# Performance work log

Hardware: AMD Instinct MI355X
Metric: run time of the kernel (lower is better)

Reference implementation:

```python
import jax, jax.numpy as jnp
import numpy as np

B, N, KD, VD, ID, H = 2, 2048, 1024, 1024, 1024, 16
HD = ID // H
SCALE = ID ** (-0.5)  # module quirk: scale uses inner_dim, not head_dim
EPS = 1e-5


def layernorm(x, g, b):
    mu = jnp.mean(x, axis=-1, keepdims=True)
    var = jnp.var(x, axis=-1, keepdims=True)
    return (x - mu) * jax.lax.rsqrt(var + EPS) * g + b


def setup_inputs() -> dict:
    key = jax.random.key(0)
    ks = jax.random.split(key, 12)
    d = {
        "keys": jax.random.normal(ks[0], (B, N, KD), jnp.float32),
        "values": jax.random.normal(ks[1], (B, N, VD), jnp.float32),
        "qk_norm_g": jnp.ones((KD,), jnp.float32),
        "qk_norm_b": jnp.zeros((KD,), jnp.float32),
        "value_norm_g": jnp.ones((VD,), jnp.float32),
        "value_norm_b": jnp.zeros((VD,), jnp.float32),
        "key_norm_g": jnp.ones((ID,), jnp.float32),
        "key_norm_b": jnp.zeros((ID,), jnp.float32),
        "query_norm_g": jnp.ones((ID,), jnp.float32),
        "query_norm_b": jnp.zeros((ID,), jnp.float32),
        "w_qk": jax.random.normal(ks[2], (KD, 2 * ID), jnp.float32) * (KD ** -0.5),
        "w_v": jax.random.normal(ks[3], (VD, ID), jnp.float32) * (VD ** -0.5),
        "w_out": jax.random.normal(ks[4], (ID, VD), jnp.float32) * (ID ** -0.5),
        "b_out": jnp.zeros((VD,), jnp.float32),
    }
    return d


def reference(keys, values, qk_norm_g, qk_norm_b, value_norm_g, value_norm_b,
              key_norm_g, key_norm_b, query_norm_g, query_norm_b,
              w_qk, w_v, w_out, b_out):
    keys = layernorm(keys, qk_norm_g, qk_norm_b)
    values = layernorm(values, value_norm_g, value_norm_b)
    qk = keys @ w_qk  # [B,N,2*ID]
    q, k = qk[..., :ID], qk[..., ID:]
    q = layernorm(q, query_norm_g, query_norm_b)
    k = layernorm(k, key_norm_g, key_norm_b)
    # b n (h d) -> b h n d
    q = q.reshape(B, N, H, HD).transpose(0, 2, 1, 3)
    k = k.reshape(B, N, H, HD).transpose(0, 2, 1, 3)
    v = (values @ w_v).reshape(B, N, H, HD).transpose(0, 2, 1, 3)
    dots = jnp.einsum('bhqd,bhkd->bhqk', q, k) * SCALE
    attn = jax.nn.softmax(dots, axis=-1)
    out = jnp.einsum('bhqk,bhkd->bhqd', attn, v)
    out = out.transpose(0, 2, 1, 3).reshape(B, N, ID)
    return out @ w_out + b_out
```

## Files before the change

### kernel.cpp

```cpp
#include <hip/hip_runtime.h>
#include <hip/hip_bf16.h>
#include <type_traits>


typedef __hip_bfloat16 bf16;
typedef __attribute__((ext_vector_type(8))) short bf16x8;
typedef __attribute__((ext_vector_type(4))) float f32x4;

#define MFMA_BF16(a, b, c) __builtin_amdgcn_mfma_f32_16x16x32_bf16((a), (b), (c), 0, 0, 0)

__device__ __forceinline__ float us2f(unsigned short u) {
  unsigned int v = ((unsigned int)u) << 16;
  return __builtin_bit_cast(float, v);
}

__device__ __forceinline__ unsigned pack_bf16x2(float a, float b) {
  union { __hip_bfloat162 h; unsigned u; } cv;
  cv.h = __float22bfloat162_rn(float2{a, b});
  return cv.u;
}

__device__ __forceinline__ unsigned pack_bf16x2_trunc(float a, float b) {
  return __builtin_amdgcn_perm(__builtin_bit_cast(unsigned, b),
                               __builtin_bit_cast(unsigned, a), 0x07060302u);
}

__device__ __forceinline__ void gl_lds16(const bf16* g, bf16* l) {
  __builtin_amdgcn_global_load_lds(
      (const __attribute__((address_space(1))) void*)g,
      (__attribute__((address_space(3))) void*)l, 16, 0, 0);
}

template <typename TIN>
__global__ __launch_bounds__(256) void ln2_kernel(
    const TIN* __restrict__ in0, const TIN* __restrict__ in1, int stride,
    const float* __restrict__ g0, const float* __restrict__ b0,
    const float* __restrict__ g1, const float* __restrict__ b1,
    bf16* __restrict__ out0, bf16* __restrict__ out1, int D,
    float sc0, float sc1)
{
  const int which = blockIdx.y;
  const TIN* in = which ? in1 : in0;
  const float* gamma = which ? g1 : g0;
  const float* beta = which ? b1 : b0;
  bf16* out = which ? out1 : out0;
  const float sc = which ? sc1 : sc0;
  const int row = blockIdx.x;
  const int t = threadIdx.x;
  float x0, x1, x2, x3;
  if constexpr (std::is_same_v<TIN, float>) {
    float4 u = *(const float4*)(in + (size_t)row * stride + t * 4);
    x0 = u.x; x1 = u.y; x2 = u.z; x3 = u.w;
  } else {
    ushort4 u = *(const ushort4*)(in + (size_t)row * stride + t * 4);
    x0 = us2f(u.x); x1 = us2f(u.y); x2 = us2f(u.z); x3 = us2f(u.w);
  }
  float s = x0 + x1 + x2 + x3;
  float s2 = x0 * x0 + x1 * x1 + x2 * x2 + x3 * x3;
#pragma unroll
  for (int m = 1; m < 64; m <<= 1) {
    s += __shfl_xor(s, m);
    s2 += __shfl_xor(s2, m);
  }
  __shared__ float red[10];
  const int w = t >> 6, lane = t & 63;
  if (lane == 0) { red[w] = s; red[4 + w] = s2; }
  __syncthreads();
  if (t == 0) {
    float S = red[0] + red[1] + red[2] + red[3];
    float S2 = red[4] + red[5] + red[6] + red[7];
    float mu = S / (float)D;
    float var = S2 / (float)D - mu * mu;
    red[8] = mu;
    red[9] = rsqrtf(var + 1e-5f);
  }
  __syncthreads();
  const float mu = red[8], rs = red[9];
  float4 g4 = *(const float4*)(gamma + t * 4);
  float4 b4 = *(const float4*)(beta + t * 4);
  uint2 o;
  o.x = pack_bf16x2(((x0 - mu) * rs * g4.x + b4.x) * sc, ((x1 - mu) * rs * g4.y + b4.y) * sc);
  o.y = pack_bf16x2(((x2 - mu) * rs * g4.z + b4.z) * sc, ((x3 - mu) * rs * g4.w + b4.w) * sc);
  *(uint2*)(out + (size_t)row * D + t * 4) = o;
}

__global__ __launch_bounds__(256) void transpose3_kernel(
    const float* __restrict__ s0, bf16* __restrict__ d0,
    const float* __restrict__ s1, bf16* __restrict__ d1,
    const float* __restrict__ s2, bf16* __restrict__ d2)
{
  const int z = blockIdx.z;
  if (z > 0 && blockIdx.x >= 16) return;
  const float* in = (z == 0) ? s0 : (z == 1) ? s1 : s2;
  bf16* out = (z == 0) ? d0 : (z == 1) ? d1 : d2;
  const int R = 1024, C = (z == 0) ? 2048 : 1024;
  __shared__ float tile[64][68];
  const int r0 = blockIdx.y * 64, c0 = blockIdx.x * 64;
  const int t = threadIdx.x;
  const int lr = t >> 2, lc = (t & 3) * 16;
  const float* src = in + (size_t)(r0 + lr) * C + (c0 + lc);
#pragma unroll
  for (int i = 0; i < 4; ++i) {
    float4 u = *(const float4*)(src + i * 4);
    tile[lr][lc + i * 4 + 0] = u.x;
    tile[lr][lc + i * 4 + 1] = u.y;
    tile[lr][lc + i * 4 + 2] = u.z;
    tile[lr][lc + i * 4 + 3] = u.w;
  }
  __syncthreads();
  __align__(16) bf16 tmp[16];
#pragma unroll
  for (int j = 0; j < 16; ++j) tmp[j] = __float2bfloat16(tile[lc + j][lr]);
  bf16* dst = out + (size_t)(c0 + lr) * R + (r0 + lc);
  *(bf16x8*)dst       = *(const bf16x8*)&tmp[0];
  *(bf16x8*)(dst + 8) = *(const bf16x8*)&tmp[8];
}

template <int BM, int BN, int TMODE, typename TOUT>
__global__ __launch_bounds__(256) void gemm_bt_kernel(
    const bf16* __restrict__ A, const bf16* __restrict__ Bt,
    const float* __restrict__ bias, TOUT* __restrict__ C,
    int M, int N, int K, int has_bias)
{
  constexpr int MT = BM / 32, NT = BN / 32;
  constexpr int ASL = BM / 32, BSL = BN / 32;
  constexpr int BUFE = (BM + BN) * 64;
  __shared__ __align__(16) bf16 smem[2 * BUFE];
  const int t = threadIdx.x;
  const int w = t >> 6, lane = t & 63, l15 = lane & 15, quad = lane >> 4;
  const int wy = w >> 1, wx = w & 1;
  const bf16* Ab = A + (size_t)blockIdx.y * BM * K;
  const bf16* Bb = Bt + (size_t)blockIdx.x * BN * K;
  f32x4 acc[MT][NT] = {};

  const bf16* aptr[ASL];
  const bf16* bptr[BSL];
#pragma unroll
  for (int i = 0; i < ASL; ++i) {
    int s = i * 256 + t, row = s >> 3, c = (s & 7) ^ (row & 7);
    aptr[i] = Ab + (size_t)row * K + (c << 3);
  }
#pragma unroll
  for (int i = 0; i < BSL; ++i) {
    int s = i * 256 + t, row = s >> 3, c = (s & 7) ^ (row & 7);
    bptr[i] = Bb + (size_t)row * K + (c << 3);
  }

  auto stage = [&](bf16* buf, int kc) {
#pragma unroll
    for (int i = 0; i < ASL; ++i)
      gl_lds16(aptr[i] + kc, buf + (i * 256 + t) * 8);
#pragma unroll
    for (int i = 0; i < BSL; ++i)
      gl_lds16(bptr[i] + kc, buf + BM * 64 + (i * 256 + t) * 8);
  };

  const int sw = (quad ^ (l15 & 7)) << 3;
  const int NK = K >> 6;

  stage(smem, 0);

  for (int kt = 0; kt < NK; ++kt) {
    const int cur = kt & 1;
    bf16* lA = smem + cur * BUFE;
    bf16* lB = lA + BM * 64;
    __builtin_amdgcn_s_barrier();
    if (kt + 1 < NK) {
      stage(smem + (cur ^ 1) * BUFE, (kt + 1) << 6);
      if constexpr (ASL + BSL == 8)
        asm volatile("s_waitcnt vmcnt(8)" ::: "memory");
      else
        asm volatile("s_waitcnt vmcnt(6)" ::: "memory");
    } else {
      asm volatile("s_waitcnt vmcnt(0)" ::: "memory");
    }
    __builtin_amdgcn_s_barrier();

#pragma unroll
    for (int h = 0; h < 2; ++h) {
      const int so = sw ^ (h << 5);
      bf16x8 af[MT], bfr[NT];
#pragma unroll
      for (int mt = 0; mt < MT; ++mt)
        af[mt] = *(const bf16x8*)&lA[(wy * (BM / 2) + mt * 16 + l15) * 64 + so];
#pragma unroll
      for (int nt = 0; nt < NT; ++nt)
        bfr[nt] = *(const bf16x8*)&lB[(wx * (BN / 2) + nt * 16 + l15) * 64 + so];
#pragma unroll
      for (int mt = 0; mt < MT; ++mt)
#pragma unroll
        for (int nt = 0; nt < NT; ++nt)
          acc[mt][nt] = MFMA_BF16(af[mt], bfr[nt], acc[mt][nt]);
    }
  }

  if constexpr (TMODE == 1) {
    static_assert(BM * BN == 8192, "TMODE1 epilogue assumes 8192 els/block");
    constexpr int STR = BM + 8;
    static_assert(BN * STR <= 2 * BUFE, "lOut must fit staging buffers");
    bf16* lOut = smem;
    __syncthreads();
#pragma unroll
    for (int mt = 0; mt < MT; ++mt)
#pragma unroll
      for (int nt = 0; nt < NT; ++nt) {
        const int d = wx * (BN / 2) + nt * 16 + l15;
        const int n = wy * (BM / 2) + mt * 16 + quad * 4;
        uint2 pk;
        pk.x = pack_bf16x2(acc[mt][nt][0], acc[mt][nt][1]);
        pk.y = pack_bf16x2(acc[mt][nt][2], acc[mt][nt][3]);
        *(uint2*)&lOut[d * STR + n] = pk;
      }
    __syncthreads();
    const int row0 = blockIdx.y * BM;
    const int bidx = row0 >> 11, n0 = row0 & 2047;
    const int col0 = blockIdx.x * BN;
    constexpr int CPR = BM / 32;
    const int d = t / CPR, off = (t % CPR) * 32;
    const bf16* srcp = &lOut[d * STR + off];
    bf16* g = (bf16*)C + ((size_t)(bidx << 10) + col0 + d) * 2048 + n0 + off;
#pragma unroll
    for (int j = 0; j < 4; ++j)
      *(bf16x8*)(g + j * 8) = *(const bf16x8*)(srcp + j * 8);
  } else {
    const int row_base = blockIdx.y * BM + wy * (BM / 2);
    const int col_base = blockIdx.x * BN + wx * (BN / 2);
#pragma unroll
    for (int mt = 0; mt < MT; ++mt)
#pragma unroll
      for (int nt = 0; nt < NT; ++nt) {
        const int col = col_base + nt * 16 + l15;
        const float bb = has_bias ? bias[col] : 0.0f;
#pragma unroll
        for (int r = 0; r < 4; ++r) {
          const int row = row_base + mt * 16 + quad * 4 + r;
          float v = acc[mt][nt][r] + bb;
          if constexpr (std::is_same_v<TOUT, bf16>)
            C[(size_t)row * N + col] = __float2bfloat16(v);
          else
            C[(size_t)row * N + col] = v;
        }
      }
  }
}

__global__ __launch_bounds__(256) void flash_kernel(
    const bf16* __restrict__ Q, const bf16* __restrict__ Km,
    const bf16* __restrict__ Vt, bf16* __restrict__ O)
{
  __shared__ __align__(16) bf16 smem[8192 + 8192 + 8192];
  bf16* lQ = smem;
  bf16* lKb = smem + 8192;
  bf16* lVb = smem + 16384;
  const int t = threadIdx.x;
  const int w = t >> 6, lane = t & 63, l15 = lane & 15, quad = lane >> 4;
  const int qt = blockIdx.x, bh = blockIdx.y;
  const int b = bh >> 4, h = bh & 15;
  const int qrow0 = b * 2048 + qt * 128;
  const bf16* qbase = Q + (size_t)qrow0 * 1024 + h * 64;
  const bf16* kbase = Km + ((size_t)(b * 2048)) * 1024 + h * 64;
  const bf16* vbase = Vt + ((size_t)(b * 1024 + h * 64)) * 2048;

  const int sr0 = t >> 3, sc0 = ((t & 7) ^ (sr0 & 7)) << 3;
  const int sr1 = (256 + t) >> 3, sc1 = (((256 + t) & 7) ^ (sr1 & 7)) << 3;
  const int gr0 = (sr0 & 0x23) | ((sr0 & 0x0C) << 1) | ((sr0 & 0x10) >> 2);
  const int gr1 = (sr1 & 0x23) | ((sr1 & 0x0C) << 1) | ((sr1 & 0x10) >> 2);
  const bf16* kp0 = kbase + gr0 * 1024 + sc0;
  const bf16* kp1 = kbase + gr1 * 1024 + sc1;
  const bf16* vp0 = vbase + sr0 * 2048 + sc0;
  const bf16* vp1 = vbase + sr1 * 2048 + sc1;

#pragma unroll
  for (int i = 0; i < 4; ++i) {
    int s = i * 256 + t;
    int row = s >> 3, c = (s & 7) ^ (row & 7);
    gl_lds16(qbase + (size_t)row * 1024 + (c << 3), lQ + s * 8);
  }
  gl_lds16(kp0, lKb + t * 8);
  gl_lds16(kp1, lKb + (256 + t) * 8);
  gl_lds16(vp0, lVb + t * 8);
  gl_lds16(vp1, lVb + (256 + t) * 8);
  asm volatile("s_waitcnt vmcnt(4)" ::: "memory");
  __builtin_amdgcn_s_barrier();

  const int sw = (quad ^ (l15 & 7)) << 3;
  bf16x8 qf[2][2];
#pragma unroll
  for (int mset = 0; mset < 2; ++mset) {
    const int row = w * 32 + mset * 16 + l15;
    qf[mset][0] = *(const bf16x8*)&lQ[row * 64 + sw];
    qf[mset][1] = *(const bf16x8*)&lQ[row * 64 + (sw ^ 32)];
  }

  f32x4 o_acc[4][2] = {};
  f32x4 l_vec[2] = {};

  for (int kt = 0; kt < 32; ++kt) {
    const int cur = kt & 1;
    bf16* lK = lKb + cur * 4096;
    bf16* lV = lVb + cur * 4096;
    bf16* lKn = lKb + (cur ^ 1) * 4096;
    bf16* lVn = lVb + (cur ^ 1) * 4096;

    __builtin_amdgcn_s_barrier();
    {
      const int ktn = (kt + 1) & 31;
      const int ko = ktn << 16;
      const int vo = ktn << 6;
      gl_lds16(kp0 + ko, lKn + t * 8);
      gl_lds16(kp1 + ko, lKn + (256 + t) * 8);
      gl_lds16(vp0 + vo, lVn + t * 8);
      gl_lds16(vp1 + vo, lVn + (256 + t) * 8);
    }
    asm volatile("s_waitcnt vmcnt(4)" ::: "memory");
    __builtin_amdgcn_s_barrier();

    bf16x8 kf[4][2];
#pragma unroll
    for (int nt = 0; nt < 4; ++nt) {
      kf[nt][0] = *(const bf16x8*)&lK[(nt * 16 + l15) * 64 + sw];
      kf[nt][1] = *(const bf16x8*)&lK[(nt * 16 + l15) * 64 + (sw ^ 32)];
    }

    bf16x8 pa[2][2];
#pragma unroll
    for (int mset = 0; mset < 2; ++mset) {
#pragma unroll
      for (int half = 0; half < 2; ++half) {
        f32x4 z0 = {}, z1 = {};
        z0 = MFMA_BF16(kf[2 * half + 0][0], qf[mset][0], z0);
        z0 = MFMA_BF16(kf[2 * half + 0][1], qf[mset][1], z0);
        z1 = MFMA_BF16(kf[2 * half + 1][0], qf[mset][0], z1);
        z1 = MFMA_BF16(kf[2 * half + 1][1], qf[mset][1], z1);
        f32x4 p0, p1;
#pragma unroll
        for (int r = 0; r < 4; ++r) {
          p0[r] = __builtin_amdgcn_exp2f(z0[r]);
          p1[r] = __builtin_amdgcn_exp2f(z1[r]);
        }
        l_vec[mset] += p0 + p1;
        union { unsigned u[4]; bf16x8 v; } cv;
        cv.u[0] = pack_bf16x2_trunc(p0[0], p0[1]);
        cv.u[1] = pack_bf16x2_trunc(p0[2], p0[3]);
        cv.u[2] = pack_bf16x2_trunc(p1[0], p1[1]);
        cv.u[3] = pack_bf16x2_trunc(p1[2], p1[3]);
        pa[mset][half] = cv.v;
      }
    }

    bf16x8 vf[4][2];
#pragma unroll
    for (int dt = 0; dt < 4; ++dt) {
      vf[dt][0] = *(const bf16x8*)&lV[(dt * 16 + l15) * 64 + sw];
      vf[dt][1] = *(const bf16x8*)&lV[(dt * 16 + l15) * 64 + (sw ^ 32)];
    }

    __builtin_amdgcn_s_setprio(1);
#pragma unroll
    for (int mset = 0; mset < 2; ++mset)
#pragma unroll
      for (int dt = 0; dt < 4; ++dt) {
        o_acc[dt][mset] = MFMA_BF16(vf[dt][0], pa[mset][0], o_acc[dt][mset]);
        o_acc[dt][mset] = MFMA_BF16(vf[dt][1], pa[mset][1], o_acc[dt][mset]);
      }
    __builtin_amdgcn_s_setprio(0);
  }

#pragma unroll
  for (int mset = 0; mset < 2; ++mset) {
    float tsum = l_vec[mset][0] + l_vec[mset][1] + l_vec[mset][2] + l_vec[mset][3];
    tsum += __shfl_xor(tsum, 16);
    tsum += __shfl_xor(tsum, 32);
    const float inv = 1.0f / tsum;
    const int m = qrow0 + w * 32 + mset * 16 + l15;
#pragma unroll
    for (int dt = 0; dt < 4; ++dt) {
      uint2 ok;
      ok.x = pack_bf16x2(o_acc[dt][mset][0] * inv, o_acc[dt][mset][1] * inv);
      ok.y = pack_bf16x2(o_acc[dt][mset][2] * inv, o_acc[dt][mset][3] * inv);
      *(uint2*)&O[(size_t)m * 1024 + h * 64 + dt * 16 + quad * 4] = ok;
    }
  }
}

extern "C" void kernel_launch(void* const* d_in, const int* in_sizes, int n_in,
                              void* d_out, int out_size, void* d_ws, size_t ws_size,
                              hipStream_t stream)
{
  (void)in_sizes; (void)n_in; (void)out_size; (void)ws_size;
  const float* keys   = (const float*)d_in[0];
  const float* values = (const float*)d_in[1];
  const float* qk_g   = (const float*)d_in[2];
  const float* qk_b   = (const float*)d_in[3];
  const float* val_g  = (const float*)d_in[4];
  const float* val_b  = (const float*)d_in[5];
  const float* key_g  = (const float*)d_in[6];
  const float* key_b  = (const float*)d_in[7];
  const float* qry_g  = (const float*)d_in[8];
  const float* qry_b  = (const float*)d_in[9];
  const float* w_qk   = (const float*)d_in[10];
  const float* w_v    = (const float*)d_in[11];
  const float* w_out  = (const float*)d_in[12];
  const float* b_out  = (const float*)d_in[13];
  float* out = (float*)d_out;

  const float CEXP = 0.03125f * 1.44269504f;

  char* ws = (char*)d_ws;
  const size_t MB = 1024 * 1024;
  bf16* keys_ln   = (bf16*)(ws + 0);
  bf16* values_ln = (bf16*)(ws + 8 * MB);
  bf16* qk        = (bf16*)(ws + 16 * MB);
  bf16* attn      = (bf16*)(ws + 16 * MB);
  bf16* vt        = (bf16*)(ws + 24 * MB);
  bf16* qln       = (bf16*)(ws + 32 * MB);
  bf16* kln       = (bf16*)(ws + 40 * MB);
  bf16* wqkT      = (bf16*)(ws + 48 * MB);
  bf16* wvT       = (bf16*)(ws + 52 * MB);
  bf16* woutT     = (bf16*)(ws + 54 * MB);

  ln2_kernel<float><<<dim3(4096, 2), 256, 0, stream>>>(
      keys, values, 1024, qk_g, qk_b, val_g, val_b, keys_ln, values_ln, 1024, 1.0f, 1.0f);
  transpose3_kernel<<<dim3(32, 16, 3), 256, 0, stream>>>(w_qk, wqkT, w_v, wvT, w_out, woutT);
  gemm_bt_kernel<128, 128, 0, bf16><<<dim3(16, 32), 256, 0, stream>>>(keys_ln, wqkT, nullptr, qk, 4096, 2048, 1024, 0);
  ln2_kernel<bf16><<<dim3(4096, 2), 256, 0, stream>>>(
      qk, qk + 1024, 2048, qry_g, qry_b, key_g, key_b, qln, kln, 1024, CEXP, 1.0f);
  gemm_bt_kernel<128, 64, 1, bf16><<<dim3(16, 32), 256, 0, stream>>>(values_ln, wvT, nullptr, vt, 4096, 1024, 1024, 0);
  flash_kernel<<<dim3(16, 32), 256, 0, stream>>>(qln, kln, vt, attn);
  gemm_bt_kernel<128, 64, 0, float><<<dim3(16, 32), 256, 0, stream>>>(attn, woutT, b_out, out, 4096, 1024, 1024, 1);
}
```

Measured before the change: 223.0 us.

## Merge prep launches and run QK and V projections in one dual GEMM

Folds the two input layernorms and the three weight transposes into a single prep kernel, and runs the QK and V projection GEMMs in one launch, with the V GEMM moved to 128x128 tiles. This cuts launch count and lets the smaller V GEMM fill the GPU alongside the QK GEMM. It also pins the barriers with sched_barrier so the compiler cannot move work across them, and repacks the workspace layout. Risks are heavier per-block shared memory in the merged kernels and schedule changes from the pinned barriers.

```diff
diff --git a/kernel.cpp b/kernel.cpp
--- a/kernel.cpp
+++ b/kernel.cpp
@@ -31,21 +31,17 @@
       (__attribute__((address_space(3))) void*)l, 16, 0, 0);
 }
 
+__device__ __forceinline__ void barrier_pinned() {
+  __builtin_amdgcn_s_barrier();
+  __builtin_amdgcn_sched_barrier(0);
+}
+
 template <typename TIN>
-__global__ __launch_bounds__(256) void ln2_kernel(
-    const TIN* __restrict__ in0, const TIN* __restrict__ in1, int stride,
-    const float* __restrict__ g0, const float* __restrict__ b0,
-    const float* __restrict__ g1, const float* __restrict__ b1,
-    bf16* __restrict__ out0, bf16* __restrict__ out1, int D,
-    float sc0, float sc1)
-{
-  const int which = blockIdx.y;
-  const TIN* in = which ? in1 : in0;
-  const float* gamma = which ? g1 : g0;
-  const float* beta = which ? b1 : b0;
-  bf16* out = which ? out1 : out0;
-  const float sc = which ? sc1 : sc0;
-  const int row = blockIdx.x;
+__device__ __forceinline__ void ln_core(
+    const TIN* __restrict__ in, const float* __restrict__ gamma,
+    const float* __restrict__ beta, bf16* __restrict__ out,
+    int stride, int D, float sc, int row, float* red)
+{
   const int t = threadIdx.x;
   float x0, x1, x2, x3;
   if constexpr (std::is_same_v<TIN, float>) {
@@ -62,7 +58,6 @@
     s += __shfl_xor(s, m);
     s2 += __shfl_xor(s2, m);
   }
-  __shared__ float red[10];
   const int w = t >> 6, lane = t & 63;
   if (lane == 0) { red[w] = s; red[4 + w] = s2; }
   __syncthreads();
@@ -84,18 +79,26 @@
   *(uint2*)(out + (size_t)row * D + t * 4) = o;
 }
 
-__global__ __launch_bounds__(256) void transpose3_kernel(
-    const float* __restrict__ s0, bf16* __restrict__ d0,
-    const float* __restrict__ s1, bf16* __restrict__ d1,
-    const float* __restrict__ s2, bf16* __restrict__ d2)
-{
-  const int z = blockIdx.z;
-  if (z > 0 && blockIdx.x >= 16) return;
-  const float* in = (z == 0) ? s0 : (z == 1) ? s1 : s2;
-  bf16* out = (z == 0) ? d0 : (z == 1) ? d1 : d2;
-  const int R = 1024, C = (z == 0) ? 2048 : 1024;
-  __shared__ float tile[64][68];
-  const int r0 = blockIdx.y * 64, c0 = blockIdx.x * 64;
+template <typename TIN>
+__global__ __launch_bounds__(256) void ln2_kernel(
+    const TIN* __restrict__ in0, const TIN* __restrict__ in1, int stride,
+    const float* __restrict__ g0, const float* __restrict__ b0,
+    const float* __restrict__ g1, const float* __restrict__ b1,
+    bf16* __restrict__ out0, bf16* __restrict__ out1, int D,
+    float sc0, float sc1)
+{
+  __shared__ float red[10];
+  const int which = blockIdx.y;
+  ln_core<TIN>(which ? in1 : in0, which ? g1 : g0, which ? b1 : b0,
+               which ? out1 : out0, stride, D, which ? sc1 : sc0,
+               blockIdx.x, red);
+}
+
+__device__ __forceinline__ void transpose_core(
+    const float* __restrict__ in, bf16* __restrict__ out, int C,
+    int r0, int c0, float (*tile)[68])
+{
+  const int R = 1024;
   const int t = threadIdx.x;
   const int lr = t >> 2, lc = (t & 3) * 16;
   const float* src = in + (size_t)(r0 + lr) * C + (c0 + lc);
@@ -116,21 +119,51 @@
   *(bf16x8*)(dst + 8) = *(const bf16x8*)&tmp[8];
 }
 
+__global__ __launch_bounds__(256) void prep_kernel(
+    const float* __restrict__ keys, const float* __restrict__ values,
+    const float* __restrict__ qk_g, const float* __restrict__ qk_b,
+    const float* __restrict__ val_g, const float* __restrict__ val_b,
+    bf16* __restrict__ keys_ln, bf16* __restrict__ values_ln,
+    const float* __restrict__ w_qk, bf16* __restrict__ wqkT,
+    const float* __restrict__ w_v, bf16* __restrict__ wvT,
+    const float* __restrict__ w_out, bf16* __restrict__ woutT)
+{
+  __shared__ float tile[64][68];
+  __shared__ float red[10];
+  const int bid = blockIdx.x;
+  if (bid < 8192) {
+    const int row = bid >> 1, which = bid & 1;
+    ln_core<float>(which ? values : keys, which ? val_g : qk_g,
+                   which ? val_b : qk_b, which ? values_ln : keys_ln,
+                   1024, 1024, 1.0f, row, red);
+  } else {
+    const int tz = bid - 8192;
+    if (tz < 512) {
+      transpose_core(w_qk, wqkT, 2048, (tz >> 5) * 64, (tz & 31) * 64, tile);
+    } else if (tz < 768) {
+      const int s = tz - 512;
+      transpose_core(w_v, wvT, 1024, (s >> 4) * 64, (s & 15) * 64, tile);
+    } else {
+      const int s = tz - 768;
+      transpose_core(w_out, woutT, 1024, (s >> 4) * 64, (s & 15) * 64, tile);
+    }
+  }
+}
+
 template <int BM, int BN, int TMODE, typename TOUT>
-__global__ __launch_bounds__(256) void gemm_bt_kernel(
+__device__ __forceinline__ void gemm_core(
     const bf16* __restrict__ A, const bf16* __restrict__ Bt,
     const float* __restrict__ bias, TOUT* __restrict__ C,
-    int M, int N, int K, int has_bias)
+    int N, int K, int has_bias, int bx, int by, bf16* smem)
 {
   constexpr int MT = BM / 32, NT = BN / 32;
   constexpr int ASL = BM / 32, BSL = BN / 32;
   constexpr int BUFE = (BM + BN) * 64;
-  __shared__ __align__(16) bf16 smem[2 * BUFE];
   const int t = threadIdx.x;
   const int w = t >> 6, lane = t & 63, l15 = lane & 15, quad = lane >> 4;
   const int wy = w >> 1, wx = w & 1;
-  const bf16* Ab = A + (size_t)blockIdx.y * BM * K;
-  const bf16* Bb = Bt + (size_t)blockIdx.x * BN * K;
+  const bf16* Ab = A + (size_t)by * BM * K;
+  const bf16* Bb = Bt + (size_t)bx * BN * K;
   f32x4 acc[MT][NT] = {};
 
   const bf16* aptr[ASL];
@@ -164,7 +197,7 @@
     const int cur = kt & 1;
     bf16* lA = smem + cur * BUFE;
     bf16* lB = lA + BM * 64;
-    __builtin_amdgcn_s_barrier();
+    barrier_pinned();
     if (kt + 1 < NK) {
       stage(smem + (cur ^ 1) * BUFE, (kt + 1) << 6);
       if constexpr (ASL + BSL == 8)
@@ -174,7 +207,7 @@
     } else {
       asm volatile("s_waitcnt vmcnt(0)" ::: "memory");
     }
-    __builtin_amdgcn_s_barrier();
+    barrier_pinned();
 
 #pragma unroll
     for (int h = 0; h < 2; ++h) {
@@ -195,7 +228,6 @@
   }
 
   if constexpr (TMODE == 1) {
-    static_assert(BM * BN == 8192, "TMODE1 epilogue assumes 8192 els/block");
     constexpr int STR = BM + 8;
     static_assert(BN * STR <= 2 * BUFE, "lOut must fit staging buffers");
     bf16* lOut = smem;
@@ -212,19 +244,24 @@
         *(uint2*)&lOut[d * STR + n] = pk;
       }
     __syncthreads();
-    const int row0 = blockIdx.y * BM;
+    const int row0 = by * BM;
     const int bidx = row0 >> 11, n0 = row0 & 2047;
-    const int col0 = blockIdx.x * BN;
+    const int col0 = bx * BN;
     constexpr int CPR = BM / 32;
-    const int d = t / CPR, off = (t % CPR) * 32;
-    const bf16* srcp = &lOut[d * STR + off];
-    bf16* g = (bf16*)C + ((size_t)(bidx << 10) + col0 + d) * 2048 + n0 + off;
-#pragma unroll
-    for (int j = 0; j < 4; ++j)
-      *(bf16x8*)(g + j * 8) = *(const bf16x8*)(srcp + j * 8);
+    constexpr int NITER = (BN * CPR) / 256;
+#pragma unroll
+    for (int it = 0; it < NITER; ++it) {
+      const int idx = it * 256 + t;
+      const int d = idx / CPR, off = (idx % CPR) * 32;
+      const bf16* srcp = &lOut[d * STR + off];
+      bf16* g = (bf16*)C + ((size_t)(bidx << 10) + col0 + d) * 2048 + n0 + off;
+#pragma unroll
+      for (int j = 0; j < 4; ++j)
+        *(bf16x8*)(g + j * 8) = *(const bf16x8*)(srcp + j * 8);
+    }
   } else {
-    const int row_base = blockIdx.y * BM + wy * (BM / 2);
-    const int col_base = blockIdx.x * BN + wx * (BN / 2);
+    const int row_base = by * BM + wy * (BM / 2);
+    const int col_base = bx * BN + wx * (BN / 2);
 #pragma unroll
     for (int mt = 0; mt < MT; ++mt)
 #pragma unroll
@@ -241,6 +278,33 @@
             C[(size_t)row * N + col] = v;
         }
       }
+  }
+}
+
+template <int BM, int BN, int TMODE, typename TOUT>
+__global__ __launch_bounds__(256) void gemm_bt_kernel(
+    const bf16* __restrict__ A, const bf16* __restrict__ Bt,
+    const float* __restrict__ bias, TOUT* __restrict__ C,
+    int N, int K, int has_bias)
+{
+  __shared__ __align__(16) bf16 smem[2 * (BM + BN) * 64];
+  gemm_core<BM, BN, TMODE, TOUT>(A, Bt, bias, C, N, K, has_bias,
+                                 blockIdx.x, blockIdx.y, smem);
+}
+
+__global__ __launch_bounds__(256) void gemm_dual_kernel(
+    const bf16* __restrict__ A0, const bf16* __restrict__ B0, bf16* __restrict__ C0,
+    const bf16* __restrict__ A1, const bf16* __restrict__ B1, bf16* __restrict__ C1)
+{
+  __shared__ __align__(16) bf16 smem[2 * 256 * 64];
+  const int bid = blockIdx.x;
+  if (bid < 512) {
+    gemm_core<128, 128, 0, bf16>(A0, B0, nullptr, C0, 2048, 1024, 0,
+                                 bid & 15, bid >> 4, smem);
+  } else {
+    const int b = bid - 512;
+    gemm_core<128, 128, 1, bf16>(A1, B1, nullptr, C1, 1024, 1024, 0,
+                                 b & 7, b >> 3, smem);
   }
 }
 
@@ -281,7 +345,7 @@
   gl_lds16(vp0, lVb + t * 8);
   gl_lds16(vp1, lVb + (256 + t) * 8);
   asm volatile("s_waitcnt vmcnt(4)" ::: "memory");
-  __builtin_amdgcn_s_barrier();
+  barrier_pinned();
 
   const int sw = (quad ^ (l15 & 7)) << 3;
   bf16x8 qf[2][2];
@@ -302,7 +366,7 @@
     bf16* lKn = lKb + (cur ^ 1) * 4096;
     bf16* lVn = lVb + (cur ^ 1) * 4096;
 
-    __builtin_amdgcn_s_barrier();
+    barrier_pinned();
     {
       const int ktn = (kt + 1) & 31;
       const int ko = ktn << 16;
@@ -313,7 +377,7 @@
       gl_lds16(vp1 + vo, lVn + (256 + t) * 8);
     }
     asm volatile("s_waitcnt vmcnt(4)" ::: "memory");
-    __builtin_amdgcn_s_barrier();
+    barrier_pinned();
 
     bf16x8 kf[4][2];
 #pragma unroll
@@ -411,21 +475,21 @@
   bf16* keys_ln   = (bf16*)(ws + 0);
   bf16* values_ln = (bf16*)(ws + 8 * MB);
   bf16* qk        = (bf16*)(ws + 16 * MB);
+  bf16* vt        = (bf16*)(ws + 32 * MB);
+  bf16* qln       = (bf16*)(ws + 0);
+  bf16* kln       = (bf16*)(ws + 8 * MB);
   bf16* attn      = (bf16*)(ws + 16 * MB);
-  bf16* vt        = (bf16*)(ws + 24 * MB);
-  bf16* qln       = (bf16*)(ws + 32 * MB);
-  bf16* kln       = (bf16*)(ws + 40 * MB);
-  bf16* wqkT      = (bf16*)(ws + 48 * MB);
-  bf16* wvT       = (bf16*)(ws + 52 * MB);
-  bf16* woutT     = (bf16*)(ws + 54 * MB);
-
-  ln2_kernel<float><<<dim3(4096, 2), 256, 0, stream>>>(
-      keys, values, 1024, qk_g, qk_b, val_g, val_b, keys_ln, values_ln, 1024, 1.0f, 1.0f);
-  transpose3_kernel<<<dim3(32, 16, 3), 256, 0, stream>>>(w_qk, wqkT, w_v, wvT, w_out, woutT);
-  gemm_bt_kernel<128, 128, 0, bf16><<<dim3(16, 32), 256, 0, stream>>>(keys_ln, wqkT, nullptr, qk, 4096, 2048, 1024, 0);
+  bf16* wqkT      = (bf16*)(ws + 40 * MB);
+  bf16* wvT       = (bf16*)(ws + 44 * MB);
+  bf16* woutT     = (bf16*)(ws + 46 * MB);
+
+  prep_kernel<<<dim3(9216), 256, 0, stream>>>(
+      keys, values, qk_g, qk_b, val_g, val_b, keys_ln, values_ln,
+      w_qk, wqkT, w_v, wvT, w_out, woutT);
+  gemm_dual_kernel<<<dim3(768), 256, 0, stream>>>(
+      keys_ln, wqkT, qk, values_ln, wvT, vt);
   ln2_kernel<bf16><<<dim3(4096, 2), 256, 0, stream>>>(
       qk, qk + 1024, 2048, qry_g, qry_b, key_g, key_b, qln, kln, 1024, CEXP, 1.0f);
-  gemm_bt_kernel<128, 64, 1, bf16><<<dim3(16, 32), 256, 0, stream>>>(values_ln, wvT, nullptr, vt, 4096, 1024, 1024, 0);
   flash_kernel<<<dim3(16, 32), 256, 0, stream>>>(qln, kln, vt, attn);
-  gemm_bt_kernel<128, 64, 0, float><<<dim3(16, 32), 256, 0, stream>>>(attn, woutT, b_out, out, 4096, 1024, 1024, 1);
-}
+  gemm_bt_kernel<128, 64, 0, float><<<dim3(16, 32), 256, 0, stream>>>(attn, woutT, b_out, out, 1024, 1024, 1);
+}
```

Result: no change. 219.5 us (-1.6%).
